# Kernel tuning notes

Hardware: AMD Instinct MI355X
Metric: run time of the kernel (lower is better)

The kernel has to match this reference:

```python
import jax, jax.numpy as jnp
import numpy as np

X_CH, Y_CH = 3, 31
C = X_CH + Y_CH            # s_channels = m_channels = 34
A = C * (C - 1) // 2       # 561 Givens rotation angles
SMIN, SMAX = 0.001, 1000.0


def setup_inputs() -> dict:
    key = jax.random.key(0)
    k1, k2 = jax.random.split(key)
    x = jax.random.normal(k1, (4, X_CH, 64, 64), dtype=jnp.float32)
    W = jax.random.normal(k2, (C + C + A, X_CH), dtype=jnp.float32) * 0.1
    b = jnp.zeros((C + C + A,), dtype=jnp.float32)
    return {"x": x, "W": W, "b": b}


def _covariance(s, a):
    # s: (B, C, H, W) positive variances; a: (B, A, H, W) rotation angles.
    B, _, H, Wd = s.shape
    cs = jnp.moveaxis(jnp.cos(a), 1, 0)  # (A, B, H, W)
    ss = jnp.moveaxis(jnp.sin(a), 1, 0)  # (A, B, H, W)
    ii, jj = np.triu_indices(C, k=1)      # same (i, j) order as the torch double loop
    ii = jnp.asarray(ii, dtype=jnp.int32)
    jj = jnp.asarray(jj, dtype=jnp.int32)

    # R starts as identity; each Givens rotation rij only mixes columns i and j
    # of R (R <- R @ rij), so we update two columns instead of a full matmul.
    R0 = jnp.broadcast_to(jnp.eye(C, dtype=s.dtype), (B, H, Wd, C, C))

    def step(R, inp):
        c_, s_, i, j = inp
        col_i = R[..., i]                      # (B, H, W, C)
        col_j = R[..., j]
        c_ = c_[..., None]
        s_ = s_[..., None]
        R = R.at[..., i].set(c_ * col_i + s_ * col_j)
        R = R.at[..., j].set(-s_ * col_i + c_ * col_j)
        return R, None

    R, _ = jax.lax.scan(step, R0, (cs, ss, ii, jj))
    sp = jnp.transpose(s, (0, 2, 3, 1))        # (B, H, W, C)
    # S = R^T D R with D = diag(sp): S[k,n] = sum_m R[m,k] * sp[m] * R[m,n]
    S = jnp.einsum('bhwmk,bhwm,bhwmn->bhwkn', R, sp, R)
    D = jnp.zeros((B, H, Wd, C, C), dtype=s.dtype).at[..., jnp.arange(C), jnp.arange(C)].set(sp)
    return S, R, D


def reference(x, W, b):
    # 1x1-conv encoder: (B, 3, H, W) -> (B, 629, H, W)
    w = jnp.einsum('oc,bchw->bohw', W, x) + b[None, :, None, None]
    m = jnp.transpose(w[:, :C], (0, 2, 3, 1))                  # (B, H, W, C) mean
    s = jax.nn.sigmoid(w[:, C:2 * C])
    s = SMIN * (1.0 - s) + SMAX * s                            # (B, C, H, W)
    a = jnp.pi * jnp.tanh(w[:, 2 * C:])                        # (B, A, H, W)
    S, _, _ = _covariance(s, a)
    return m, S, s
```

## Files before the change

kernel.cpp:

```cpp
#include <hip/hip_runtime.h>


#define CCH 34
#define ACH 561
#define HWPIX 4096
#define NPIX 16384
#define PXB 7
#define NTHR 128
#define CLEN 141
#define CSPX (CLEN * 8)
#define VROW 36
#define VPX (17 * VROW * 4)
#define OFF_S 557056
#define OFF_s 19496960
#define LOG2E 1.4426950408889634f

typedef float    f32x2 __attribute__((ext_vector_type(2)));
typedef _Float16 h2    __attribute__((ext_vector_type(2)));

struct Pairs {
    short i[ACH]; short j[ACH];
    constexpr Pairs() : i(), j() {
        int p = 0;
        for (int a = 0; a < CCH - 1; ++a)
            for (int b = a + 1; b < CCH; ++b) { i[p] = (short)a; j[p] = (short)b; ++p; }
    }
};
__device__ constexpr Pairs PR{};

__device__ __forceinline__ float dot2h(h2 a, h2 b, float c) {
#if __has_builtin(__builtin_amdgcn_fdot2)
    return __builtin_amdgcn_fdot2(a, b, c, false);
#else
    return fmaf((float)a[0], (float)b[0], fmaf((float)a[1], (float)b[1], c));
#endif
}

__device__ __forceinline__ void rot2(f32x2& Ri, f32x2& Rj, f32x2 c2, f32x2 s2) {
    f32x2 t1 = s2 * Rj;
    f32x2 t2 = s2 * Ri;
    Ri = __builtin_elementwise_fma(c2, Ri, t1);
    Rj = __builtin_elementwise_fma(c2, Rj, -t2);
}

template <int P0, int P1>
__device__ __forceinline__ void apply_rots(f32x2* R2, const char* csb) {
    #pragma unroll
    for (int k = P0; k < P1; ++k) {
        f32x2 cell = *(const f32x2*)(csb + (k - P0) * 8);
        f32x2 c2 = __builtin_shufflevector(cell, cell, 0, 0);
        f32x2 s2 = __builtin_shufflevector(cell, cell, 1, 1);
        rot2(R2[PR.i[k]], R2[PR.j[k]], c2, s2);
    }
}

__device__ __forceinline__ float2 cs_of(float wv) {
    float e  = __builtin_amdgcn_exp2f((2.0f * LOG2E) * wv);
    float tt = 1.0f - 2.0f * __builtin_amdgcn_rcpf(e + 1.0f);
    float rv = 0.5f * tt;
    return make_float2(__builtin_amdgcn_cosf(rv), __builtin_amdgcn_sinf(rv));
}

template <int G0, int LEN>
__device__ __forceinline__ void fill_cs(const float* __restrict__ Wm,
                                        const float* __restrict__ bvec,
                                        const float* xs, char* csbuf,
                                        int npx, int t) {
    for (int o = t; o < npx * LEN; o += NTHR) {
        int px = (int)((unsigned)o / (unsigned)LEN);
        int l  = o - px * LEN;
        int ch = 2 * CCH + G0 + l;
        float wv = fmaf(Wm[ch*3+0], xs[px*3+0],
                   fmaf(Wm[ch*3+1], xs[px*3+1], Wm[ch*3+2] * xs[px*3+2])) + bvec[ch];
        *(float2*)(csbuf + px * CSPX + l * 8) = cs_of(wv);
    }
}

__global__ __launch_bounds__(NTHR, 4) void gpd_kernel(
    const float* __restrict__ x,
    const float* __restrict__ Wm,
    const float* __restrict__ bvec,
    float* __restrict__ out)
{
    __shared__ alignas(16) char vbuf[PXB * VPX];
    __shared__ _Float16 lds_sh[PXB * CCH];
    __shared__ float xs[PXB * 3];

    const int t   = threadIdx.x;
    const int p0  = blockIdx.x * PXB;
    const int npx = min(PXB, NPIX - p0);

    for (int i = t; i < npx * 3; i += NTHR) {
        int px = (int)((unsigned)i / 3u); int c = i - px * 3;
        int p = p0 + px; int b = p >> 12; int hw = p & 4095;
        xs[i] = x[(b * 3 + c) * HWPIX + hw];
    }
    __syncthreads();

    for (int o = t; o < npx * 68; o += NTHR) {
        int q = (int)((unsigned)o / 68u); int ch = o - q * 68;
        int p = p0 + q; int b = p >> 12; int hw = p & 4095;
        float wv = fmaf(Wm[ch*3+0], xs[q*3+0],
                   fmaf(Wm[ch*3+1], xs[q*3+1], Wm[ch*3+2] * xs[q*3+2])) + bvec[ch];
        if (ch < CCH) {
            out[(size_t)p * CCH + ch] = wv;
        } else {
            float e  = __builtin_amdgcn_exp2f(-wv * LOG2E);
            float sg = __builtin_amdgcn_rcpf(1.0f + e);
            float sv = fmaf(999.999f, sg, 0.001f);
            int c = ch - CCH;
            out[OFF_s + (size_t)(b * CCH + c) * HWPIX + hw] = sv;
            lds_sh[q * CCH + c] = (_Float16)sv;
        }
    }

    const int px = t / 17;
    const int u  = t - px * 17;
    const bool act = (px < npx);
    const char* csb = vbuf + px * CSPX;

    f32x2 R2[CCH];
    #pragma unroll
    for (int n = 0; n < CCH; ++n) {
        R2[n][0] = (n == 2 * u)     ? 1.0f : 0.0f;
        R2[n][1] = (n == 2 * u + 1) ? 1.0f : 0.0f;
    }

    fill_cs<0, 141>(Wm, bvec, xs, vbuf, npx, t);
    __syncthreads();
    if (act) apply_rots<0, 141>(R2, csb);
    __syncthreads();
    fill_cs<141, 140>(Wm, bvec, xs, vbuf, npx, t);
    __syncthreads();
    if (act) apply_rots<141, 281>(R2, csb);
    __syncthreads();
    fill_cs<281, 140>(Wm, bvec, xs, vbuf, npx, t);
    __syncthreads();
    if (act) apply_rots<281, 421>(R2, csb);
    __syncthreads();
    fill_cs<421, 140>(Wm, bvec, xs, vbuf, npx, t);
    __syncthreads();
    if (act) apply_rots<421, 561>(R2, csb);
    __syncthreads();

    if (act) {
        unsigned* vb = (unsigned*)(vbuf + px * VPX) + u * VROW;
        #pragma unroll
        for (int n = 0; n < CCH; ++n)
            vb[n] = __builtin_bit_cast(unsigned,
                        __builtin_amdgcn_cvt_pkrtz(R2[n][0], R2[n][1]));
    }
    __syncthreads();

    if (act) {
        const unsigned* vb = (const unsigned*)(vbuf + px * VPX);
        const _Float16* sh = lds_sh + px * CCH;
        float aL[CCH], aH[CCH];
        #pragma unroll
        for (int n = 0; n < CCH; ++n) { aL[n] = 0.0f; aH[n] = 0.0f; }
        for (int mp = 0; mp < 17; ++mp) {
            const unsigned* row = vb + mp * VROW;
            h2 sh2 = *(const h2*)(sh + 2 * mp);
            h2 vkL = __builtin_bit_cast(h2, row[2 * u])     * sh2;
            h2 vkH = __builtin_bit_cast(h2, row[2 * u + 1]) * sh2;
            #pragma unroll
            for (int g = 0; g < 8; ++g) {
                uint4 rr = *(const uint4*)(row + 4 * g);
                h2 r0 = __builtin_bit_cast(h2, rr.x), r1 = __builtin_bit_cast(h2, rr.y);
                h2 r2 = __builtin_bit_cast(h2, rr.z), r3 = __builtin_bit_cast(h2, rr.w);
                aL[4*g+0] = dot2h(vkL, r0, aL[4*g+0]);  aH[4*g+0] = dot2h(vkH, r0, aH[4*g+0]);
                aL[4*g+1] = dot2h(vkL, r1, aL[4*g+1]);  aH[4*g+1] = dot2h(vkH, r1, aH[4*g+1]);
                aL[4*g+2] = dot2h(vkL, r2, aL[4*g+2]);  aH[4*g+2] = dot2h(vkH, r2, aH[4*g+2]);
                aL[4*g+3] = dot2h(vkL, r3, aL[4*g+3]);  aH[4*g+3] = dot2h(vkH, r3, aH[4*g+3]);
            }
            uint2 rr2 = *(const uint2*)(row + 32);
            h2 r32 = __builtin_bit_cast(h2, rr2.x), r33 = __builtin_bit_cast(h2, rr2.y);
            aL[32] = dot2h(vkL, r32, aL[32]);  aH[32] = dot2h(vkH, r32, aH[32]);
            aL[33] = dot2h(vkL, r33, aL[33]);  aH[33] = dot2h(vkH, r33, aH[33]);
        }
        float* os = out + OFF_S + (size_t)(p0 + px) * (CCH * CCH) + 2 * u * CCH;
        #pragma unroll
        for (int q = 0; q < 17; ++q) {
            float4 v;
            v.x = (4*q+0 < 34) ? aL[4*q+0] : aH[4*q+0-34];
            v.y = (4*q+1 < 34) ? aL[4*q+1] : aH[4*q+1-34];
            v.z = (4*q+2 < 34) ? aL[4*q+2] : aH[4*q+2-34];
            v.w = (4*q+3 < 34) ? aL[4*q+3] : aH[4*q+3-34];
            *(float4*)(os + 4 * q) = v;
        }
    }
}

extern "C" void kernel_launch(void* const* d_in, const int* in_sizes, int n_in,
                              void* d_out, int out_size, void* d_ws, size_t ws_size,
                              hipStream_t stream) {
    const float* x  = (const float*)d_in[0];
    const float* W  = (const float*)d_in[1];
    const float* bv = (const float*)d_in[2];
    float* out = (float*)d_out;
    const int nblk = (NPIX + PXB - 1) / PXB;
    hipLaunchKernelGGL(gpd_kernel, dim3(nblk), dim3(NTHR), 0, stream,
                       x, W, bv, out);
}
```

Measured before the change: 74.74 us.

## Process 14 pixels per block with 9 threads each holding four R columns

Each thread now tracks four columns of the rotation matrix (two f32x2 banks) instead of two, so 9 threads per pixel cover 34 columns and a 128-thread block handles 14 pixels. Each loaded cos/sin pair is reused across twice as many rotations. The S = R^T D R stage runs in two halves of 7 pixels, reusing the same LDS buffer, with R kept in registers as packed halves between the halves. The cost is doubled register pressure (launch bounds lowered to 2 blocks per SIMD), extra barriers, and more LDS for the cos/sin buffer of 14 pixels.

```diff
diff --git a/kernel.cpp b/kernel.cpp
--- a/kernel.cpp
+++ b/kernel.cpp
@@ -5,10 +5,10 @@
 #define ACH 561
 #define HWPIX 4096
 #define NPIX 16384
-#define PXB 7
+#define PXB 14
+#define TPP 9
 #define NTHR 128
-#define CLEN 141
-#define CSPX (CLEN * 8)
+#define CSPX (141 * 8)
 #define VROW 36
 #define VPX (17 * VROW * 4)
 #define OFF_S 557056
@@ -18,15 +18,15 @@
 typedef float    f32x2 __attribute__((ext_vector_type(2)));
 typedef _Float16 h2    __attribute__((ext_vector_type(2)));
 
-struct Pairs {
+struct PairsT {
     short i[ACH]; short j[ACH];
-    constexpr Pairs() : i(), j() {
+    constexpr PairsT() : i(), j() {
         int p = 0;
         for (int a = 0; a < CCH - 1; ++a)
             for (int b = a + 1; b < CCH; ++b) { i[p] = (short)a; j[p] = (short)b; ++p; }
     }
 };
-__device__ constexpr Pairs PR{};
+__device__ constexpr PairsT PR{};
 
 __device__ __forceinline__ float dot2h(h2 a, h2 b, float c) {
 #if __has_builtin(__builtin_amdgcn_fdot2)
@@ -36,21 +36,25 @@
 #endif
 }
 
-__device__ __forceinline__ void rot2(f32x2& Ri, f32x2& Rj, f32x2 c2, f32x2 s2) {
-    f32x2 t1 = s2 * Rj;
-    f32x2 t2 = s2 * Ri;
-    Ri = __builtin_elementwise_fma(c2, Ri, t1);
-    Rj = __builtin_elementwise_fma(c2, Rj, -t2);
+__device__ __forceinline__ void rot4(f32x2& Rai, f32x2& Raj,
+                                     f32x2& Rbi, f32x2& Rbj,
+                                     f32x2 c2, f32x2 s2) {
+    f32x2 ta = s2 * Rai;
+    f32x2 tb = s2 * Rbi;
+    Rai = __builtin_elementwise_fma(c2, Rai, s2 * Raj);
+    Rbi = __builtin_elementwise_fma(c2, Rbi, s2 * Rbj);
+    Raj = __builtin_elementwise_fma(c2, Raj, -ta);
+    Rbj = __builtin_elementwise_fma(c2, Rbj, -tb);
 }
 
 template <int P0, int P1>
-__device__ __forceinline__ void apply_rots(f32x2* R2, const char* csb) {
+__device__ __forceinline__ void apply_rots(f32x2* Ra, f32x2* Rb, const char* csb) {
     #pragma unroll
     for (int k = P0; k < P1; ++k) {
         f32x2 cell = *(const f32x2*)(csb + (k - P0) * 8);
         f32x2 c2 = __builtin_shufflevector(cell, cell, 0, 0);
         f32x2 s2 = __builtin_shufflevector(cell, cell, 1, 1);
-        rot2(R2[PR.i[k]], R2[PR.j[k]], c2, s2);
+        rot4(Ra[PR.i[k]], Ra[PR.j[k]], Rb[PR.i[k]], Rb[PR.j[k]], c2, s2);
     }
 }
 
@@ -76,13 +80,13 @@
     }
 }
 
-__global__ __launch_bounds__(NTHR, 4) void gpd_kernel(
+__global__ __launch_bounds__(NTHR, 2) void gpd_kernel(
     const float* __restrict__ x,
     const float* __restrict__ Wm,
     const float* __restrict__ bvec,
     float* __restrict__ out)
 {
-    __shared__ alignas(16) char vbuf[PXB * VPX];
+    __shared__ alignas(16) char vbuf[7 * VPX];
     __shared__ _Float16 lds_sh[PXB * CCH];
     __shared__ float xs[PXB * 3];
 
@@ -114,80 +118,102 @@
         }
     }
 
-    const int px = t / 17;
-    const int u  = t - px * 17;
-    const bool act = (px < npx);
+    const int px = t / TPP;
+    const int u  = t - px * TPP;
+    const bool act = (t < PXB * TPP) && (px < npx);
     const char* csb = vbuf + px * CSPX;
 
-    f32x2 R2[CCH];
+    f32x2 Ra[CCH], Rb[CCH];
     #pragma unroll
     for (int n = 0; n < CCH; ++n) {
-        R2[n][0] = (n == 2 * u)     ? 1.0f : 0.0f;
-        R2[n][1] = (n == 2 * u + 1) ? 1.0f : 0.0f;
+        Ra[n][0] = (n == 4 * u)     ? 1.0f : 0.0f;
+        Ra[n][1] = (n == 4 * u + 1) ? 1.0f : 0.0f;
+        Rb[n][0] = (n == 4 * u + 2) ? 1.0f : 0.0f;
+        Rb[n][1] = (n == 4 * u + 3) ? 1.0f : 0.0f;
     }
 
     fill_cs<0, 141>(Wm, bvec, xs, vbuf, npx, t);
     __syncthreads();
-    if (act) apply_rots<0, 141>(R2, csb);
+    if (act) apply_rots<0, 141>(Ra, Rb, csb);
     __syncthreads();
     fill_cs<141, 140>(Wm, bvec, xs, vbuf, npx, t);
     __syncthreads();
-    if (act) apply_rots<141, 281>(R2, csb);
+    if (act) apply_rots<141, 281>(Ra, Rb, csb);
     __syncthreads();
     fill_cs<281, 140>(Wm, bvec, xs, vbuf, npx, t);
     __syncthreads();
-    if (act) apply_rots<281, 421>(R2, csb);
+    if (act) apply_rots<281, 421>(Ra, Rb, csb);
     __syncthreads();
     fill_cs<421, 140>(Wm, bvec, xs, vbuf, npx, t);
     __syncthreads();
-    if (act) apply_rots<421, 561>(R2, csb);
-    __syncthreads();
-
-    if (act) {
-        unsigned* vb = (unsigned*)(vbuf + px * VPX) + u * VROW;
-        #pragma unroll
-        for (int n = 0; n < CCH; ++n)
-            vb[n] = __builtin_bit_cast(unsigned,
-                        __builtin_amdgcn_cvt_pkrtz(R2[n][0], R2[n][1]));
-    }
-    __syncthreads();
-
-    if (act) {
-        const unsigned* vb = (const unsigned*)(vbuf + px * VPX);
-        const _Float16* sh = lds_sh + px * CCH;
-        float aL[CCH], aH[CCH];
-        #pragma unroll
-        for (int n = 0; n < CCH; ++n) { aL[n] = 0.0f; aH[n] = 0.0f; }
-        for (int mp = 0; mp < 17; ++mp) {
-            const unsigned* row = vb + mp * VROW;
-            h2 sh2 = *(const h2*)(sh + 2 * mp);
-            h2 vkL = __builtin_bit_cast(h2, row[2 * u])     * sh2;
-            h2 vkH = __builtin_bit_cast(h2, row[2 * u + 1]) * sh2;
+    if (act) apply_rots<421, 561>(Ra, Rb, csb);
+    __syncthreads();
+
+    unsigned RhA[CCH], RhB[CCH];
+    #pragma unroll
+    for (int n = 0; n < CCH; ++n) {
+        RhA[n] = __builtin_bit_cast(unsigned,
+                     __builtin_amdgcn_cvt_pkrtz(Ra[n][0], Ra[n][1]));
+        RhB[n] = __builtin_bit_cast(unsigned,
+                     __builtin_amdgcn_cvt_pkrtz(Rb[n][0], Rb[n][1]));
+    }
+
+    const int cpx = t / 18;
+    const int u2  = t - cpx * 18;
+
+    #pragma unroll
+    for (int h = 0; h < 2; ++h) {
+        const int lr = px - 7 * h;
+        if (act && lr >= 0 && lr < 7) {
+            unsigned* vbw = (unsigned*)(vbuf + lr * VPX);
             #pragma unroll
-            for (int g = 0; g < 8; ++g) {
-                uint4 rr = *(const uint4*)(row + 4 * g);
-                h2 r0 = __builtin_bit_cast(h2, rr.x), r1 = __builtin_bit_cast(h2, rr.y);
-                h2 r2 = __builtin_bit_cast(h2, rr.z), r3 = __builtin_bit_cast(h2, rr.w);
-                aL[4*g+0] = dot2h(vkL, r0, aL[4*g+0]);  aH[4*g+0] = dot2h(vkH, r0, aH[4*g+0]);
-                aL[4*g+1] = dot2h(vkL, r1, aL[4*g+1]);  aH[4*g+1] = dot2h(vkH, r1, aH[4*g+1]);
-                aL[4*g+2] = dot2h(vkL, r2, aL[4*g+2]);  aH[4*g+2] = dot2h(vkH, r2, aH[4*g+2]);
-                aL[4*g+3] = dot2h(vkL, r3, aL[4*g+3]);  aH[4*g+3] = dot2h(vkH, r3, aH[4*g+3]);
+            for (int n = 0; n < CCH; ++n) vbw[(2*u)*VROW + n] = RhA[n];
+            if (u < 8) {
+                #pragma unroll
+                for (int n = 0; n < CCH; ++n) vbw[(2*u+1)*VROW + n] = RhB[n];
             }
-            uint2 rr2 = *(const uint2*)(row + 32);
-            h2 r32 = __builtin_bit_cast(h2, rr2.x), r33 = __builtin_bit_cast(h2, rr2.y);
-            aL[32] = dot2h(vkL, r32, aL[32]);  aH[32] = dot2h(vkH, r32, aH[32]);
-            aL[33] = dot2h(vkL, r33, aL[33]);  aH[33] = dot2h(vkH, r33, aH[33]);
         }
-        float* os = out + OFF_S + (size_t)(p0 + px) * (CCH * CCH) + 2 * u * CCH;
-        #pragma unroll
-        for (int q = 0; q < 17; ++q) {
-            float4 v;
-            v.x = (4*q+0 < 34) ? aL[4*q+0] : aH[4*q+0-34];
-            v.y = (4*q+1 < 34) ? aL[4*q+1] : aH[4*q+1-34];
-            v.z = (4*q+2 < 34) ? aL[4*q+2] : aH[4*q+2-34];
-            v.w = (4*q+3 < 34) ? aL[4*q+3] : aH[4*q+3-34];
-            *(float4*)(os + 4 * q) = v;
+        __syncthreads();
+
+        const int gpx = 7 * h + cpx;
+        if (t < 126 && u2 < 17 && gpx < npx) {
+            const unsigned* vb = (const unsigned*)(vbuf + cpx * VPX);
+            const _Float16* shp = lds_sh + gpx * CCH;
+            float aL[CCH], aH[CCH];
+            #pragma unroll
+            for (int n = 0; n < CCH; ++n) { aL[n] = 0.0f; aH[n] = 0.0f; }
+            for (int w = 0; w < 17; ++w) {
+                const unsigned* row = vb + w * VROW;
+                h2 sh2 = *(const h2*)(shp + 2 * w);
+                h2 vkL = __builtin_bit_cast(h2, row[2 * u2])     * sh2;
+                h2 vkH = __builtin_bit_cast(h2, row[2 * u2 + 1]) * sh2;
+                #pragma unroll
+                for (int g = 0; g < 8; ++g) {
+                    uint4 rr = *(const uint4*)(row + 4 * g);
+                    h2 r0 = __builtin_bit_cast(h2, rr.x), r1 = __builtin_bit_cast(h2, rr.y);
+                    h2 r2 = __builtin_bit_cast(h2, rr.z), r3 = __builtin_bit_cast(h2, rr.w);
+                    aL[4*g+0] = dot2h(vkL, r0, aL[4*g+0]);  aH[4*g+0] = dot2h(vkH, r0, aH[4*g+0]);
+                    aL[4*g+1] = dot2h(vkL, r1, aL[4*g+1]);  aH[4*g+1] = dot2h(vkH, r1, aH[4*g+1]);
+                    aL[4*g+2] = dot2h(vkL, r2, aL[4*g+2]);  aH[4*g+2] = dot2h(vkH, r2, aH[4*g+2]);
+                    aL[4*g+3] = dot2h(vkL, r3, aL[4*g+3]);  aH[4*g+3] = dot2h(vkH, r3, aH[4*g+3]);
+                }
+                uint2 rr2 = *(const uint2*)(row + 32);
+                h2 r32 = __builtin_bit_cast(h2, rr2.x), r33 = __builtin_bit_cast(h2, rr2.y);
+                aL[32] = dot2h(vkL, r32, aL[32]);  aH[32] = dot2h(vkH, r32, aH[32]);
+                aL[33] = dot2h(vkL, r33, aL[33]);  aH[33] = dot2h(vkH, r33, aH[33]);
+            }
+            float* os = out + OFF_S + (size_t)(p0 + gpx) * (CCH * CCH) + 2 * u2 * CCH;
+            #pragma unroll
+            for (int q = 0; q < 17; ++q) {
+                float4 v;
+                v.x = (4*q+0 < 34) ? aL[4*q+0] : aH[4*q+0-34];
+                v.y = (4*q+1 < 34) ? aL[4*q+1] : aH[4*q+1-34];
+                v.z = (4*q+2 < 34) ? aL[4*q+2] : aH[4*q+2-34];
+                v.w = (4*q+3 < 34) ? aL[4*q+3] : aH[4*q+3-34];
+                *(float4*)(os + 4 * q) = v;
+            }
         }
+        __syncthreads();
     }
 }
 
```

After: 94.74 us. +26.8%, slower.
